# Optimization experiments

Hardware: AMD Instinct MI355X
Metric: run time of the kernel (lower is better)

Reference implementation:

```python
import jax, jax.numpy as jnp
import numpy as np

N = 4096   # number of simplices at each order
D = 1024   # in_relations (feature width)


def setup_inputs() -> dict:
    key = jax.random.key(0)
    ks = jax.random.split(key, 8)
    H = jax.random.normal(ks[0], (N, D), dtype=jnp.float32)
    H_low = jax.random.normal(ks[1], (N, D), dtype=jnp.float32)
    H_high = jax.random.normal(ks[2], (N, D), dtype=jnp.float32)
    L = jax.random.normal(ks[3], (N, N), dtype=jnp.float32)       # Laplacian (same order)
    B_low = jax.random.normal(ks[4], (N, N), dtype=jnp.float32)   # boundary, shape [N_low, N]
    B_high = jax.random.normal(ks[5], (N, N), dtype=jnp.float32)  # boundary, shape [N, N_high]
    W = jax.random.normal(ks[6], (D, 3 * D), dtype=jnp.float32) * 0.02  # torch Linear weight [out, in]
    b = jnp.zeros((D,), dtype=jnp.float32)
    return {"L": L, "H": H, "B_low": B_low, "H_low": H_low,
            "B_high": B_high, "H_high": H_high, "W": W, "b": b}


def _simplicial_attn(Hq, KV, mask):
    # scores: [Nq, Nkv]; double softmax with mask-multiply in between
    scale = 1.0 / np.sqrt(Hq.shape[1]).astype(np.float32)
    s = jnp.matmul(Hq, KV.T) * scale
    a = jax.nn.softmax(s, axis=1)
    a = jax.nn.softmax(a * mask, axis=1)
    return jnp.matmul(a, KV)


def reference(L, H, B_low, H_low, B_high, H_high, W, b):
    dt = H.dtype
    m_same = (L != 0).astype(dt)                 # [N, N]
    m_low = (B_low != 0).T.astype(dt)            # [N, N_low]
    m_high = (B_high != 0).astype(dt)            # [N, N_high]
    H1 = _simplicial_attn(H, H, m_same)
    H2 = _simplicial_attn(H, H_low, m_low)
    H3 = _simplicial_attn(H, H_high, m_high)
    H4 = jnp.concatenate((H1, H2, H3), axis=1)   # [N, 3D]
    return jnp.tanh(jnp.matmul(H4, W.T) + b)
```

## Files before the change

kernel.cpp:

```cpp
#include <hip/hip_runtime.h>


typedef unsigned short u16;
typedef unsigned int u32;
typedef __attribute__((ext_vector_type(8))) short short8;
typedef __attribute__((ext_vector_type(4))) float floatx4;

#define NS 4096
#define DF 1024

__device__ __forceinline__ u16 f2b(float x) {
    u32 u = __float_as_uint(x);
    u32 r = (u + 0x7fffu + ((u >> 16) & 1u)) >> 16;
    return (u16)r;
}
__device__ __forceinline__ u32 packb(float a, float b) {
    return (u32)f2b(a) | ((u32)f2b(b) << 16);
}
__device__ __forceinline__ void unpack8(uint4 u, float* v) {
    v[0] = __uint_as_float(u.x << 16); v[1] = __uint_as_float(u.x & 0xffff0000u);
    v[2] = __uint_as_float(u.y << 16); v[3] = __uint_as_float(u.y & 0xffff0000u);
    v[4] = __uint_as_float(u.z << 16); v[5] = __uint_as_float(u.z & 0xffff0000u);
    v[6] = __uint_as_float(u.w << 16); v[7] = __uint_as_float(u.w & 0xffff0000u);
}

struct GemmDesc {
    const u16* A; const u16* B; void* C;
    const float* bias;
    int K, lda, ldb, ldc, nTilesX, nTilesY, nBlocks, colMajor, epi;
    float alpha;
};

__device__ __forceinline__ void stage_tile(
    const u16* __restrict__ Ab, const u16* __restrict__ Bb,
    int lda, int ldb, int kt, u16* as, u16* bs, int tid)
{
    const int wave = tid >> 6;
#pragma unroll
    for (int i = 0; i < 4; i++) {
        int chunk = i * 512 + tid;
        int row   = chunk >> 3;
        int l     = (chunk & 7) ^ (row & 7);
        const u16* ga = Ab + (size_t)row * lda + kt + l * 8;
        __builtin_amdgcn_global_load_lds(
            (const __attribute__((address_space(1))) void*)ga,
            (__attribute__((address_space(3))) void*)&as[(i * 512 + wave * 64) * 8],
            16, 0, 0);
    }
#pragma unroll
    for (int i = 0; i < 4; i++) {
        int chunk = i * 512 + tid;
        int row   = chunk >> 3;
        int l     = (chunk & 7) ^ (row & 7);
        const u16* gb = Bb + (size_t)row * ldb + kt + l * 8;
        __builtin_amdgcn_global_load_lds(
            (const __attribute__((address_space(1))) void*)gb,
            (__attribute__((address_space(3))) void*)&bs[(i * 512 + wave * 64) * 8],
            16, 0, 0);
    }
}

__global__ __launch_bounds__(512, 2)
void mgemm8(GemmDesc d0, GemmDesc d1, GemmDesc d2, GemmDesc d3)
{
    __shared__ u16 As[2][256 * 64];
    __shared__ u16 Bs[2][256 * 64];

    int bid = blockIdx.x;
    const GemmDesc* d;
    if (bid < d0.nBlocks) d = &d0;
    else {
        bid -= d0.nBlocks;
        if (bid < d1.nBlocks) d = &d1;
        else {
            bid -= d1.nBlocks;
            if (bid < d2.nBlocks) d = &d2;
            else { bid -= d2.nBlocks; d = &d3; }
        }
    }

    const int tid  = threadIdx.x;
    const int wave = tid >> 6;
    const int lane = tid & 63;
    const int wm = wave >> 2, wn = wave & 3;
    const int q = lane >> 4, r16 = lane & 15;

    int bm, bn;
    if (d->colMajor) { bm = bid % d->nTilesY; bn = bid / d->nTilesY; }
    else             { bn = bid % d->nTilesX; bm = bid / d->nTilesX; }

    const u16* Ab = d->A + (size_t)bm * 256 * d->lda;
    const u16* Bb = d->B + (size_t)bn * 256 * d->ldb;
    const int lda = d->lda, ldb = d->ldb;

    floatx4 acc[8][4];
#pragma unroll
    for (int i = 0; i < 8; i++)
#pragma unroll
        for (int j = 0; j < 4; j++) acc[i][j] = (floatx4){0.f, 0.f, 0.f, 0.f};

    stage_tile(Ab, Bb, lda, ldb, 0, As[0], Bs[0], tid);

    const int nkt = d->K >> 6;
    for (int t = 0; t < nkt; ++t) {
        u16* as = As[t & 1];
        u16* bs = Bs[t & 1];
        if (t + 1 < nkt) {
            stage_tile(Ab, Bb, lda, ldb, (t + 1) << 6, As[(t + 1) & 1], Bs[(t + 1) & 1], tid);
            asm volatile("s_waitcnt vmcnt(8)" ::: "memory");
        } else {
            asm volatile("s_waitcnt vmcnt(0)" ::: "memory");
        }
        __builtin_amdgcn_sched_barrier(0);
        __builtin_amdgcn_s_barrier();
        asm volatile("" ::: "memory");
        __builtin_amdgcn_sched_barrier(0);

        short8 bq[4][2];
#pragma unroll
        for (int ni = 0; ni < 4; ni++)
#pragma unroll
            for (int kk = 0; kk < 2; kk++) {
                int row  = wn * 64 + ni * 16 + r16;
                int phys = (kk * 4 + q) ^ (row & 7);
                bq[ni][kk] = *(const short8*)&bs[row * 64 + phys * 8];
            }
#pragma unroll
        for (int p = 0; p < 4; p++) {
            short8 af[2][2];
#pragma unroll
            for (int m2 = 0; m2 < 2; m2++)
#pragma unroll
                for (int kk = 0; kk < 2; kk++) {
                    int row  = wm * 128 + (p * 2 + m2) * 16 + r16;
                    int phys = (kk * 4 + q) ^ (row & 7);
                    af[m2][kk] = *(const short8*)&as[row * 64 + phys * 8];
                }
            __builtin_amdgcn_s_setprio(1);
#pragma unroll
            for (int m2 = 0; m2 < 2; m2++)
#pragma unroll
                for (int ni = 0; ni < 4; ni++)
#pragma unroll
                    for (int kk = 0; kk < 2; kk++)
                        acc[p * 2 + m2][ni] = __builtin_amdgcn_mfma_f32_16x16x32_bf16(
                            af[m2][kk], bq[ni][kk], acc[p * 2 + m2][ni], 0, 0, 0);
            __builtin_amdgcn_s_setprio(0);
        }
        asm volatile("s_waitcnt lgkmcnt(0)" ::: "memory");
        __builtin_amdgcn_sched_barrier(0);
        __builtin_amdgcn_s_barrier();
        asm volatile("" ::: "memory");
        __builtin_amdgcn_sched_barrier(0);
    }

    const int ldc = d->ldc;
#pragma unroll
    for (int mi = 0; mi < 8; mi++) {
#pragma unroll
        for (int ni = 0; ni < 4; ni++) {
            floatx4 v = acc[mi][ni];
            int col  = bn * 256 + wn * 64 + ni * 16 + r16;
            int rowb = bm * 256 + wm * 128 + mi * 16 + q * 4;
            if (d->epi == 0) {
                u16* C = (u16*)d->C;
#pragma unroll
                for (int r = 0; r < 4; r++)
                    C[(size_t)(rowb + r) * ldc + col] = f2b(v[r] * d->alpha);
            } else {
                float* C = (float*)d->C;
#pragma unroll
                for (int r = 0; r < 4; r++)
                    C[(size_t)(rowb + r) * ldc + col] = v[r];
            }
        }
    }
}

struct SmDesc { u16* S; const float* mF; const u32* mB; };

__device__ __forceinline__ float blockMax(float x, volatile float* red) {
#pragma unroll
    for (int off = 32; off > 0; off >>= 1) x = fmaxf(x, __shfl_xor(x, off, 64));
    __syncthreads();
    if ((threadIdx.x & 63) == 0) red[threadIdx.x >> 6] = x;
    __syncthreads();
    return fmaxf(fmaxf(red[0], red[1]), fmaxf(red[2], red[3]));
}
__device__ __forceinline__ float blockSum(float x, volatile float* red) {
#pragma unroll
    for (int off = 32; off > 0; off >>= 1) x += __shfl_xor(x, off, 64);
    __syncthreads();
    if ((threadIdx.x & 63) == 0) red[threadIdx.x >> 6] = x;
    __syncthreads();
    return red[0] + red[1] + red[2] + red[3];
}

__global__ __launch_bounds__(256)
void dsoftmax3(SmDesc d0, SmDesc d1, SmDesc d2, int ldS)
{
    __shared__ float red[4];
    const int bid = blockIdx.x;
    const int br  = bid >> 12;
    const int row = bid & 4095;
    const SmDesc d = (br == 0) ? d0 : (br == 1) ? d1 : d2;
    u16* Srow = d.S + (size_t)row * ldS;
    const int t = threadIdx.x;

    float v[16];
    uint4 u0 = ((const uint4*)Srow)[t * 2];
    uint4 u1 = ((const uint4*)Srow)[t * 2 + 1];
    unpack8(u0, v); unpack8(u1, v + 8);

    float m = -1e30f;
#pragma unroll
    for (int j = 0; j < 16; j++) m = fmaxf(m, v[j]);
    m = blockMax(m, red);

    float s = 0.f;
#pragma unroll
    for (int j = 0; j < 16; j++) { v[j] = __expf(v[j] - m); s += v[j]; }
    s = blockSum(s, red);
    float rz = 1.0f / s;

    float v2[16];
    if (d.mF) {
        const float* mrow = d.mF + (size_t)row * NS;
#pragma unroll
        for (int k = 0; k < 4; k++) {
            float4 mv = ((const float4*)mrow)[t * 4 + k];
            v2[k * 4 + 0] = (mv.x != 0.f) ? v[k * 4 + 0] * rz : 0.f;
            v2[k * 4 + 1] = (mv.y != 0.f) ? v[k * 4 + 1] * rz : 0.f;
            v2[k * 4 + 2] = (mv.z != 0.f) ? v[k * 4 + 2] * rz : 0.f;
            v2[k * 4 + 3] = (mv.w != 0.f) ? v[k * 4 + 3] * rz : 0.f;
        }
    } else {
        u32 w = d.mB[(size_t)row * (NS / 32) + (t >> 1)];
        u32 half = (w >> ((t & 1) * 16)) & 0xffffu;
#pragma unroll
        for (int j = 0; j < 16; j++)
            v2[j] = ((half >> j) & 1u) ? v[j] * rz : 0.f;
    }

    float m2 = -1e30f;
#pragma unroll
    for (int j = 0; j < 16; j++) m2 = fmaxf(m2, v2[j]);
    m2 = blockMax(m2, red);
    float s2 = 0.f;
#pragma unroll
    for (int j = 0; j < 16; j++) { v2[j] = __expf(v2[j] - m2); s2 += v2[j]; }
    s2 = blockSum(s2, red);
    float rz2 = 1.0f / s2;

    uint4 o0, o1;
    o0.x = packb(v2[0] * rz2,  v2[1] * rz2);
    o0.y = packb(v2[2] * rz2,  v2[3] * rz2);
    o0.z = packb(v2[4] * rz2,  v2[5] * rz2);
    o0.w = packb(v2[6] * rz2,  v2[7] * rz2);
    o1.x = packb(v2[8] * rz2,  v2[9] * rz2);
    o1.y = packb(v2[10] * rz2, v2[11] * rz2);
    o1.z = packb(v2[12] * rz2, v2[13] * rz2);
    o1.w = packb(v2[14] * rz2, v2[15] * rz2);
    ((uint4*)Srow)[t * 2]     = o0;
    ((uint4*)Srow)[t * 2 + 1] = o1;
}

__global__ __launch_bounds__(256)
void cvt_h3(const float* __restrict__ X0, const float* __restrict__ X1,
            const float* __restrict__ X2, u16* __restrict__ Y)
{
    const float* X = (blockIdx.z == 0) ? X0 : (blockIdx.z == 1) ? X1 : X2;
    u16* Yb = Y + (size_t)blockIdx.z * NS * DF;
    int i = blockIdx.x * 256 + threadIdx.x;
    float4 x = ((const float4*)X)[i];
    ushort4 y;
    y.x = f2b(x.x); y.y = f2b(x.y); y.z = f2b(x.z); y.w = f2b(x.w);
    ((ushort4*)Yb)[i] = y;
}

__global__ __launch_bounds__(256)
void mask_bits(const float* __restrict__ X, u32* __restrict__ MT, int n)
{
    __shared__ float tile[32][33];
    const int tx = threadIdx.x, ty = threadIdx.y;
    const int bx = blockIdx.x * 32, by = blockIdx.y * 32;
#pragma unroll
    for (int k = 0; k < 4; k++) {
        int r = by + ty + k * 8;
        tile[ty + k * 8][tx] = X[(size_t)r * n + bx + tx];
    }
    __syncthreads();
#pragma unroll
    for (int k = 0; k < 4; k++) {
        int c = bx + ty + k * 8;
        unsigned long long m = __ballot(tile[tx][ty + k * 8] != 0.f);
        u32 w = (ty & 1) ? (u32)(m >> 32) : (u32)m;
        if (tx == 0) MT[(size_t)c * (n / 32) + (by >> 5)] = w;
    }
}

__global__ __launch_bounds__(256)
void cvtk(const float* __restrict__ X, u16* __restrict__ Y, int n4)
{
    int i = blockIdx.x * 256 + threadIdx.x;
    if (i >= n4) return;
    float4 x = ((const float4*)X)[i];
    ushort4 y;
    y.x = f2b(x.x); y.y = f2b(x.y); y.z = f2b(x.z); y.w = f2b(x.w);
    ((ushort4*)Y)[i] = y;
}

__global__ __launch_bounds__(256)
void combine4(const float* __restrict__ P1, const float* __restrict__ P2,
              const float* __restrict__ P3, const float* __restrict__ bias,
              float* __restrict__ out)
{
    int i = blockIdx.x * 256 + threadIdx.x;
    float4 a = ((const float4*)out)[i];
    float4 b = ((const float4*)P1)[i];
    float4 c = ((const float4*)P2)[i];
    float4 e = ((const float4*)P3)[i];
    float4 bb = ((const float4*)bias)[i & 255];
    float4 o;
    o.x = tanhf(a.x + b.x + c.x + e.x + bb.x);
    o.y = tanhf(a.y + b.y + c.y + e.y + bb.y);
    o.z = tanhf(a.z + b.z + c.z + e.z + bb.z);
    o.w = tanhf(a.w + b.w + c.w + e.w + bb.w);
    ((float4*)out)[i] = o;
}

static inline GemmDesc mk8(const u16* A, const u16* B, void* C,
                           int K, int lda, int ldb, int ldc,
                           int nTX, int nTY, int epi, float alpha,
                           int colMajor)
{
    GemmDesc d;
    d.A = A; d.B = B; d.C = C; d.bias = nullptr;
    d.K = K; d.lda = lda; d.ldb = ldb; d.ldc = ldc;
    d.nTilesX = nTX; d.nTilesY = nTY; d.nBlocks = nTX * nTY;
    d.colMajor = colMajor; d.epi = epi; d.alpha = alpha;
    return d;
}

extern "C" void kernel_launch(void* const* d_in, const int* in_sizes, int n_in,
                              void* d_out, int out_size, void* d_ws, size_t ws_size,
                              hipStream_t stream)
{
    const float* L      = (const float*)d_in[0];
    const float* H      = (const float*)d_in[1];
    const float* B_low  = (const float*)d_in[2];
    const float* H_low  = (const float*)d_in[3];
    const float* B_high = (const float*)d_in[4];
    const float* H_high = (const float*)d_in[5];
    const float* W      = (const float*)d_in[6];
    const float* bvec   = (const float*)d_in[7];
    float* out = (float*)d_out;

    const size_t MB = 1024 * 1024;
    char* ws = (char*)d_ws;
    dim3 bt(32, 8);

    u16* S    = (u16*)(ws + 0);
    u16* Hcat = (u16*)(ws + 96 * MB);
    u16* Wb   = (u16*)(ws + 120 * MB);
    u32* mlT  = (u32*)(ws + 126 * MB);
    u16* GT   = (u16*)(ws + 128 * MB);
    float* P1 = (float*)(ws + 96 * MB);
    float* P2 = (float*)(ws + 112 * MB);
    float* P3 = (float*)(ws + 152 * MB);

    cvt_h3<<<dim3(NS * DF / 4 / 256, 1, 3), 256, 0, stream>>>(H, H_low, H_high, Hcat);
    cvtk<<<(DF * 3 * DF / 4 + 255) / 256, 256, 0, stream>>>(W, Wb, DF * 3 * DF / 4);
    mask_bits<<<dim3(NS / 32, NS / 32), bt, 0, stream>>>(B_low, mlT, NS);

    GemmDesc sg = mk8(Hcat, Hcat, S, DF, DF, DF, 3 * NS,
                      3 * NS / 256, NS / 256, 0, 0.03125f, 1);
    GemmDesc g0 = mk8(Wb,          Hcat,               GT,          DF, 3 * DF, DF, 3 * NS, NS / 256, DF / 256, 0, 1.0f, 1);
    GemmDesc g1 = mk8(Wb + DF,     Hcat + NS * DF,     GT + NS,     DF, 3 * DF, DF, 3 * NS, NS / 256, DF / 256, 0, 1.0f, 1);
    GemmDesc g2 = mk8(Wb + 2 * DF, Hcat + 2 * NS * DF, GT + 2 * NS, DF, 3 * DF, DF, 3 * NS, NS / 256, DF / 256, 0, 1.0f, 1);
    mgemm8<<<sg.nBlocks + g0.nBlocks + g1.nBlocks + g2.nBlocks, 512, 0, stream>>>(sg, g0, g1, g2);

    SmDesc s0 = {S,          L,       nullptr};
    SmDesc s1 = {S + NS,     nullptr, mlT};
    SmDesc s2 = {S + 2 * NS, B_high,  nullptr};
    dsoftmax3<<<3 * NS, 256, 0, stream>>>(s0, s1, s2, 3 * NS);

    GemmDesc f0 = mk8(S,          GT,          out, 3 * DF, 3 * NS, 3 * NS, DF, DF / 256, NS / 256, 1, 1.0f, 1);
    GemmDesc f1 = mk8(S + 3 * DF, GT + 3 * DF, P1,  3 * DF, 3 * NS, 3 * NS, DF, DF / 256, NS / 256, 1, 1.0f, 1);
    GemmDesc f2 = mk8(S + 6 * DF, GT + 6 * DF, P2,  3 * DF, 3 * NS, 3 * NS, DF, DF / 256, NS / 256, 1, 1.0f, 1);
    GemmDesc f3 = mk8(S + 9 * DF, GT + 9 * DF, P3,  3 * DF, 3 * NS, 3 * NS, DF, DF / 256, NS / 256, 1, 1.0f, 1);
    mgemm8<<<f0.nBlocks + f1.nBlocks + f2.nBlocks + f3.nBlocks, 512, 0, stream>>>(f0, f1, f2, f3);

    combine4<<<NS * DF / 4 / 256, 256, 0, stream>>>(P1, P2, P3, bvec, out);
}
```

Baseline: 537.5 us.

## Split GEMM tile staging into half-tiles interleaved with MFMA quads

The bf16 MFMA GEMM mainloop no longer stages a whole 256x64 A/B tile per iteration. It now loads 128-row half-tiles spread across four MFMA sub-phases, each separated by barriers. B is prefetched two k-steps ahead into the buffer just consumed, and A one step ahead. The aim is to overlap global-to-LDS traffic with compute more evenly and shorten the stalls at iteration boundaries. In exchange it adds more barriers per iteration and depends on delicate vmcnt/lgkmcnt bookkeeping, which risks races or extra synchronisation overhead.

```diff
diff --git a/kernel.cpp b/kernel.cpp
--- a/kernel.cpp
+++ b/kernel.cpp
@@ -8,6 +8,7 @@
 
 #define NS 4096
 #define DF 1024
+#define HS (128 * 64)
 
 __device__ __forceinline__ u16 f2b(float x) {
     u32 u = __float_as_uint(x);
@@ -31,40 +32,65 @@
     float alpha;
 };
 
-__device__ __forceinline__ void stage_tile(
-    const u16* __restrict__ Ab, const u16* __restrict__ Bb,
-    int lda, int ldb, int kt, u16* as, u16* bs, int tid)
-{
-    const int wave = tid >> 6;
-#pragma unroll
-    for (int i = 0; i < 4; i++) {
+__device__ __forceinline__ void stage_half(
+    const u16* __restrict__ gsrc,
+    int ld, u16* dst, int tid)
+{
+    const int wbase = (tid >> 6) * 64;
+#pragma unroll
+    for (int i = 0; i < 2; i++) {
         int chunk = i * 512 + tid;
         int row   = chunk >> 3;
         int l     = (chunk & 7) ^ (row & 7);
-        const u16* ga = Ab + (size_t)row * lda + kt + l * 8;
+        const u16* g = gsrc + (size_t)row * ld + l * 8;
         __builtin_amdgcn_global_load_lds(
-            (const __attribute__((address_space(1))) void*)ga,
-            (__attribute__((address_space(3))) void*)&as[(i * 512 + wave * 64) * 8],
+            (const __attribute__((address_space(1))) void*)g,
+            (__attribute__((address_space(3))) void*)&dst[(i * 512 + wbase) * 8],
             16, 0, 0);
     }
-#pragma unroll
-    for (int i = 0; i < 4; i++) {
-        int chunk = i * 512 + tid;
-        int row   = chunk >> 3;
-        int l     = (chunk & 7) ^ (row & 7);
-        const u16* gb = Bb + (size_t)row * ldb + kt + l * 8;
-        __builtin_amdgcn_global_load_lds(
-            (const __attribute__((address_space(1))) void*)gb,
-            (__attribute__((address_space(3))) void*)&bs[(i * 512 + wave * 64) * 8],
-            16, 0, 0);
-    }
+}
+
+__device__ __forceinline__ void read_af(const u16* aw, int quad, int r16, int q,
+                                        short8 af[2][2])
+{
+#pragma unroll
+    for (int m2 = 0; m2 < 2; m2++)
+#pragma unroll
+        for (int kk = 0; kk < 2; kk++) {
+            int lr   = (quad * 2 + m2) * 16 + r16;
+            int phys = (kk * 4 + q) ^ (lr & 7);
+            af[m2][kk] = *(const short8*)&aw[lr * 64 + phys * 8];
+        }
+}
+__device__ __forceinline__ void mfma_quad(int quad, const short8 af[2][2],
+                                          const short8 bq[4][2], floatx4 acc[8][4])
+{
+#pragma unroll
+    for (int m2 = 0; m2 < 2; m2++)
+#pragma unroll
+        for (int ni = 0; ni < 4; ni++)
+#pragma unroll
+            for (int kk = 0; kk < 2; kk++)
+                acc[quad * 2 + m2][ni] = __builtin_amdgcn_mfma_f32_16x16x32_bf16(
+                    af[m2][kk], bq[ni][kk], acc[quad * 2 + m2][ni], 0, 0, 0);
+}
+
+__device__ __forceinline__ void pre_mfma() {
+    __builtin_amdgcn_s_barrier();
+    asm volatile("s_waitcnt lgkmcnt(0)" ::: "memory");
+    __builtin_amdgcn_sched_barrier(0);
+    __builtin_amdgcn_s_setprio(1);
+}
+__device__ __forceinline__ void post_mfma() {
+    __builtin_amdgcn_s_setprio(0);
+    __builtin_amdgcn_sched_barrier(0);
 }
 
 __global__ __launch_bounds__(512, 2)
 void mgemm8(GemmDesc d0, GemmDesc d1, GemmDesc d2, GemmDesc d3)
 {
-    __shared__ u16 As[2][256 * 64];
-    __shared__ u16 Bs[2][256 * 64];
+    __shared__ u16 As[4 * HS];
+    __shared__ u16 Bs[4 * HS];
 
     int bid = blockIdx.x;
     const GemmDesc* d;
@@ -80,8 +106,8 @@
     }
 
     const int tid  = threadIdx.x;
+    const int lane = tid & 63;
     const int wave = tid >> 6;
-    const int lane = tid & 63;
     const int wm = wave >> 2, wn = wave & 3;
     const int q = lane >> 4, r16 = lane & 15;
 
@@ -92,6 +118,7 @@
     const u16* Ab = d->A + (size_t)bm * 256 * d->lda;
     const u16* Bb = d->B + (size_t)bn * 256 * d->ldb;
     const int lda = d->lda, ldb = d->ldb;
+    const int nkt = d->K >> 6;
 
     floatx4 acc[8][4];
 #pragma unroll
@@ -99,59 +126,57 @@
 #pragma unroll
         for (int j = 0; j < 4; j++) acc[i][j] = (floatx4){0.f, 0.f, 0.f, 0.f};
 
-    stage_tile(Ab, Bb, lda, ldb, 0, As[0], Bs[0], tid);
-
-    const int nkt = d->K >> 6;
+    stage_half(Bb,                          ldb, Bs + 0 * HS, tid);
+    stage_half(Bb + (size_t)128 * ldb,      ldb, Bs + 1 * HS, tid);
+    stage_half(Ab,                          lda, As + 0 * HS, tid);
+    stage_half(Ab + (size_t)128 * lda,      lda, As + 1 * HS, tid);
+    stage_half(Bb + 64,                     ldb, Bs + 2 * HS, tid);
+    stage_half(Bb + (size_t)128 * ldb + 64, ldb, Bs + 3 * HS, tid);
+    asm volatile("s_waitcnt vmcnt(4)" ::: "memory");
+    __builtin_amdgcn_s_barrier();
+
     for (int t = 0; t < nkt; ++t) {
-        u16* as = As[t & 1];
-        u16* bs = Bs[t & 1];
-        if (t + 1 < nkt) {
-            stage_tile(Ab, Bb, lda, ldb, (t + 1) << 6, As[(t + 1) & 1], Bs[(t + 1) & 1], tid);
-            asm volatile("s_waitcnt vmcnt(8)" ::: "memory");
-        } else {
-            asm volatile("s_waitcnt vmcnt(0)" ::: "memory");
-        }
-        __builtin_amdgcn_sched_barrier(0);
+        const int cur = t & 1, nxt = cur ^ 1;
+        const u16* aw = As + (cur * 2 + wm) * HS;
+        const u16* bw = Bs + (cur * 2 + (wn >> 1)) * HS;
+        const int kt1 = (t + 1) << 6;
+        const int kt2 = (t + 2) << 6;
+        short8 bq[4][2], af[2][2];
+
+#pragma unroll
+        for (int ni = 0; ni < 4; ni++)
+#pragma unroll
+            for (int kk = 0; kk < 2; kk++) {
+                int lrb  = (wn & 1) * 64 + ni * 16 + r16;
+                int phys = (kk * 4 + q) ^ (lrb & 7);
+                bq[ni][kk] = *(const short8*)&bw[lrb * 64 + phys * 8];
+            }
+        read_af(aw, 0, r16, q, af);
+        if (t + 1 < nkt)
+            stage_half(Ab + kt1, lda, As + (nxt * 2 + 0) * HS, tid);
+        asm volatile("s_waitcnt lgkmcnt(8)" ::: "memory");
+        pre_mfma(); mfma_quad(0, af, bq, acc); post_mfma();
         __builtin_amdgcn_s_barrier();
-        asm volatile("" ::: "memory");
-        __builtin_amdgcn_sched_barrier(0);
-
-        short8 bq[4][2];
-#pragma unroll
-        for (int ni = 0; ni < 4; ni++)
-#pragma unroll
-            for (int kk = 0; kk < 2; kk++) {
-                int row  = wn * 64 + ni * 16 + r16;
-                int phys = (kk * 4 + q) ^ (row & 7);
-                bq[ni][kk] = *(const short8*)&bs[row * 64 + phys * 8];
-            }
-#pragma unroll
-        for (int p = 0; p < 4; p++) {
-            short8 af[2][2];
-#pragma unroll
-            for (int m2 = 0; m2 < 2; m2++)
-#pragma unroll
-                for (int kk = 0; kk < 2; kk++) {
-                    int row  = wm * 128 + (p * 2 + m2) * 16 + r16;
-                    int phys = (kk * 4 + q) ^ (row & 7);
-                    af[m2][kk] = *(const short8*)&as[row * 64 + phys * 8];
-                }
-            __builtin_amdgcn_s_setprio(1);
-#pragma unroll
-            for (int m2 = 0; m2 < 2; m2++)
-#pragma unroll
-                for (int ni = 0; ni < 4; ni++)
-#pragma unroll
-                    for (int kk = 0; kk < 2; kk++)
-                        acc[p * 2 + m2][ni] = __builtin_amdgcn_mfma_f32_16x16x32_bf16(
-                            af[m2][kk], bq[ni][kk], acc[p * 2 + m2][ni], 0, 0, 0);
-            __builtin_amdgcn_s_setprio(0);
-        }
-        asm volatile("s_waitcnt lgkmcnt(0)" ::: "memory");
-        __builtin_amdgcn_sched_barrier(0);
+
+        read_af(aw, 1, r16, q, af);
+        if (t + 1 < nkt)
+            stage_half(Ab + (size_t)128 * lda + kt1, lda, As + (nxt * 2 + 1) * HS, tid);
+        if (t + 2 < nkt)
+            stage_half(Bb + kt2, ldb, Bs + (cur * 2 + 0) * HS, tid);
+        pre_mfma(); mfma_quad(1, af, bq, acc); post_mfma();
         __builtin_amdgcn_s_barrier();
-        asm volatile("" ::: "memory");
-        __builtin_amdgcn_sched_barrier(0);
+
+        read_af(aw, 2, r16, q, af);
+        if (t + 2 < nkt)
+            stage_half(Bb + (size_t)128 * ldb + kt2, ldb, Bs + (cur * 2 + 1) * HS, tid);
+        pre_mfma(); mfma_quad(2, af, bq, acc); post_mfma();
+        __builtin_amdgcn_s_barrier();
+
+        read_af(aw, 3, r16, q, af);
+        pre_mfma(); mfma_quad(3, af, bq, acc); post_mfma();
+        if (t == nkt - 2)      asm volatile("s_waitcnt vmcnt(0)" ::: "memory");
+        else if (t < nkt - 2)  asm volatile("s_waitcnt vmcnt(4)" ::: "memory");
+        __builtin_amdgcn_s_barrier();
     }
 
     const int ldc = d->ldc;
```

Result: faster. 525.7 us (-2.2%).

## Restructure GEMM main loop to load all fragments before issuing next-tile prefetch

Applied to the files above, without the earlier changes.

The K-loop now reads every A and B fragment for the current tile from LDS into registers up front. Only after that does it issue the global-to-LDS staging of the next tile, and then it runs all MFMAs in two k-halves. This drops the mid-loop vmcnt wait and one of the two barriers per iteration, so the prefetch can overlap with the matrix math. The cost is more live registers (8x2 A fragments held at once), which may reduce occupancy or cause spills.

```diff
diff --git a/kernel.cpp b/kernel.cpp
--- a/kernel.cpp
+++ b/kernel.cpp
@@ -80,8 +80,8 @@
     }
 
     const int tid  = threadIdx.x;
+    const int lane = tid & 63;
     const int wave = tid >> 6;
-    const int lane = tid & 63;
     const int wm = wave >> 2, wn = wave & 3;
     const int q = lane >> 4, r16 = lane & 15;
 
@@ -92,6 +92,7 @@
     const u16* Ab = d->A + (size_t)bm * 256 * d->lda;
     const u16* Bb = d->B + (size_t)bn * 256 * d->ldb;
     const int lda = d->lda, ldb = d->ldb;
+    const int nkt = d->K >> 6;
 
     floatx4 acc[8][4];
 #pragma unroll
@@ -100,58 +101,54 @@
         for (int j = 0; j < 4; j++) acc[i][j] = (floatx4){0.f, 0.f, 0.f, 0.f};
 
     stage_tile(Ab, Bb, lda, ldb, 0, As[0], Bs[0], tid);
-
-    const int nkt = d->K >> 6;
+    __syncthreads();
+
     for (int t = 0; t < nkt; ++t) {
-        u16* as = As[t & 1];
-        u16* bs = Bs[t & 1];
-        if (t + 1 < nkt) {
-            stage_tile(Ab, Bb, lda, ldb, (t + 1) << 6, As[(t + 1) & 1], Bs[(t + 1) & 1], tid);
-            asm volatile("s_waitcnt vmcnt(8)" ::: "memory");
-        } else {
-            asm volatile("s_waitcnt vmcnt(0)" ::: "memory");
-        }
-        __builtin_amdgcn_sched_barrier(0);
-        __builtin_amdgcn_s_barrier();
-        asm volatile("" ::: "memory");
-        __builtin_amdgcn_sched_barrier(0);
-
-        short8 bq[4][2];
-#pragma unroll
-        for (int ni = 0; ni < 4; ni++)
-#pragma unroll
-            for (int kk = 0; kk < 2; kk++) {
+        const int cur = t & 1, nxt = cur ^ 1;
+        const u16* aw = As[cur];
+        const u16* bw = Bs[cur];
+        short8 af[8][2], bq[4][2];
+
+#pragma unroll
+        for (int kk = 0; kk < 2; kk++) {
+#pragma unroll
+            for (int ni = 0; ni < 4; ni++) {
                 int row  = wn * 64 + ni * 16 + r16;
                 int phys = (kk * 4 + q) ^ (row & 7);
-                bq[ni][kk] = *(const short8*)&bs[row * 64 + phys * 8];
+                bq[ni][kk] = *(const short8*)&bw[row * 64 + phys * 8];
             }
 #pragma unroll
-        for (int p = 0; p < 4; p++) {
-            short8 af[2][2];
-#pragma unroll
-            for (int m2 = 0; m2 < 2; m2++)
-#pragma unroll
-                for (int kk = 0; kk < 2; kk++) {
-                    int row  = wm * 128 + (p * 2 + m2) * 16 + r16;
-                    int phys = (kk * 4 + q) ^ (row & 7);
-                    af[m2][kk] = *(const short8*)&as[row * 64 + phys * 8];
-                }
-            __builtin_amdgcn_s_setprio(1);
-#pragma unroll
-            for (int m2 = 0; m2 < 2; m2++)
-#pragma unroll
-                for (int ni = 0; ni < 4; ni++)
-#pragma unroll
-                    for (int kk = 0; kk < 2; kk++)
-                        acc[p * 2 + m2][ni] = __builtin_amdgcn_mfma_f32_16x16x32_bf16(
-                            af[m2][kk], bq[ni][kk], acc[p * 2 + m2][ni], 0, 0, 0);
-            __builtin_amdgcn_s_setprio(0);
+            for (int mi = 0; mi < 8; mi++) {
+                int row  = wm * 128 + mi * 16 + r16;
+                int phys = (kk * 4 + q) ^ (row & 7);
+                af[mi][kk] = *(const short8*)&aw[row * 64 + phys * 8];
+            }
         }
-        asm volatile("s_waitcnt lgkmcnt(0)" ::: "memory");
+        if (t + 1 < nkt)
+            stage_tile(Ab, Bb, lda, ldb, (t + 1) << 6, As[nxt], Bs[nxt], tid);
         __builtin_amdgcn_sched_barrier(0);
-        __builtin_amdgcn_s_barrier();
-        asm volatile("" ::: "memory");
+
+        __builtin_amdgcn_s_setprio(1);
+#pragma unroll
+        for (int mi = 0; mi < 8; mi++)
+#pragma unroll
+            for (int ni = 0; ni < 4; ni++)
+                acc[mi][ni] = __builtin_amdgcn_mfma_f32_16x16x32_bf16(
+                    af[mi][0], bq[ni][0], acc[mi][ni], 0, 0, 0);
+        __builtin_amdgcn_s_setprio(0);
         __builtin_amdgcn_sched_barrier(0);
+
+        __builtin_amdgcn_s_setprio(1);
+#pragma unroll
+        for (int mi = 0; mi < 8; mi++)
+#pragma unroll
+            for (int ni = 0; ni < 4; ni++)
+                acc[mi][ni] = __builtin_amdgcn_mfma_f32_16x16x32_bf16(
+                    af[mi][1], bq[ni][1], acc[mi][ni], 0, 0, 0);
+        __builtin_amdgcn_s_setprio(0);
+        __builtin_amdgcn_sched_barrier(0);
+
+        if (t + 1 < nkt) __syncthreads();
     }
 
     const int ldc = d->ldc;
```

Measured after the change: 501.7 us. 1.07x faster.
